# Performance work log

Hardware: AMD Instinct MI355X
Metric: run time of the kernel (lower is better)

The kernel has to match this reference:

```python
import jax, jax.numpy as jnp
import numpy as np

EPS = 1e-05


def project_to_poincare_ball(v, eps=EPS):
    # clip norm to < 1 - eps
    norm = jnp.linalg.norm(v, axis=-1, keepdims=True)
    scale = jnp.minimum((1.0 - eps) / (norm + 1e-10), 1.0)
    return v * scale


def setup_inputs() -> dict:
    key = jax.random.key(0)
    k1, k2 = jax.random.split(key)
    B, S, D, V = 2, 2048, 512, 32000
    # scale by 0.02 so typical norms (~0.45) lie inside the unit ball
    hidden_states = jax.random.normal(k1, (B, S, D), dtype=jnp.float32) * 0.02
    weight = jax.random.normal(k2, (V, D), dtype=jnp.float32) * 0.02
    return {"hidden_states": hidden_states, "weight": weight}


def reference(hidden_states, weight):
    eps = EPS
    B, S, D = hidden_states.shape
    x = hidden_states.reshape(-1, D)                 # (N, D)
    x = project_to_poincare_ball(x, eps)
    y = project_to_poincare_ball(weight, eps)        # (V, D)

    x_norm_sq = jnp.sum(x * x, axis=-1, keepdims=True)   # (N, 1)
    y_norm_sq = jnp.sum(y * y, axis=-1)                  # (V,)

    # torch.cdist(p=2, use_mm_for_euclid_dist): ||x-y|| via mm expansion,
    # clamped at 0 before sqrt. NOTE: original code names this diff_norm_sq
    # but it is the (unsquared) distance -- reproduced faithfully.
    sq = x_norm_sq + y_norm_sq[None, :] - 2.0 * (x @ y.T)   # (N, V)
    dist = jnp.sqrt(jnp.maximum(sq, 0.0))

    denom = (1.0 - x_norm_sq) * (1.0 - y_norm_sq)[None, :]  # (N, V)
    argument = 1.0 + 2.0 * dist / (denom + eps)
    argument = jnp.maximum(argument, 1.0 + eps)
    distances = jnp.arccosh(argument)                       # (N, V)

    logits = -distances
    return logits.reshape(B, S, -1)
```

## Files before the change

kernel.cpp:

```cpp
#include <hip/hip_runtime.h>
#include <hip/hip_bf16.h>

#define D_DIM 512
#define EPS 1e-5f
#define BM 256
#define BN 128
#define BK 32
#define KT 16
#define SLOT_SHORTS (BM * BK + BN * BK)

typedef __attribute__((ext_vector_type(8))) short bf16x8;
typedef __attribute__((ext_vector_type(4))) float f32x4;

__device__ __forceinline__ unsigned short f2bf(float f) {
  unsigned int u = __float_as_uint(f);
  u += 0x7FFFu + ((u >> 16) & 1u);
  return (unsigned short)(u >> 16);
}

__global__ __launch_bounds__(256) void prep_rows2(
    const float* __restrict__ x, const float* __restrict__ w,
    unsigned short* __restrict__ Xbf, unsigned short* __restrict__ Ybf,
    float* __restrict__ xnsq, float* __restrict__ ynsq, int N, int total)
{
  int row  = blockIdx.x * 4 + (threadIdx.x >> 6);
  int lane = threadIdx.x & 63;
  if (row >= total) return;

  const float* src; unsigned short* dst; float* nsq; int r;
  if (row < N) { src = x; dst = Xbf; nsq = xnsq; r = row; }
  else         { src = w; dst = Ybf; nsq = ynsq; r = row - N; }

  const float4* s = (const float4*)(src + (size_t)r * D_DIM);
  float4 v0 = s[lane];
  float4 v1 = s[lane + 64];
  float ss = v0.x*v0.x + v0.y*v0.y + v0.z*v0.z + v0.w*v0.w
           + v1.x*v1.x + v1.y*v1.y + v1.z*v1.z + v1.w*v1.w;
  #pragma unroll
  for (int off = 32; off; off >>= 1) ss += __shfl_xor(ss, off);

  float norm  = sqrtf(ss);
  float scale = fminf((1.0f - EPS) / (norm + 1e-10f), 1.0f);
  if (lane == 0) nsq[r] = ss * scale * scale;

  ushort4 o0, o1;
  o0.x = f2bf(v0.x * scale); o0.y = f2bf(v0.y * scale);
  o0.z = f2bf(v0.z * scale); o0.w = f2bf(v0.w * scale);
  o1.x = f2bf(v1.x * scale); o1.y = f2bf(v1.y * scale);
  o1.z = f2bf(v1.z * scale); o1.w = f2bf(v1.w * scale);

  ushort4* dp = (ushort4*)(dst + (size_t)r * D_DIM);
  dp[lane]      = o0;
  dp[lane + 64] = o1;
}

__global__ __launch_bounds__(512, 4) void hyp_gemm(
    const unsigned short* __restrict__ Xbf, const unsigned short* __restrict__ Ybf,
    const float* __restrict__ xnsq, const float* __restrict__ ynsq,
    float* __restrict__ out, int N, int V)
{
  __shared__ __attribute__((aligned(16))) unsigned short sAB[3][SLOT_SHORTS];

  int bid = blockIdx.x;
  int local = bid >> 3;
  int bn = local >> 1;
  int bm = (bid & 7) * 2 + (local & 1);

  int tid  = threadIdx.x;
  int wid  = tid >> 6;
  int lane = tid & 63;
  int wm = wid >> 1, wn = wid & 1;

  size_t a_row0 = (size_t)bm * BM;
  size_t b_row0 = (size_t)bn * BN;

  auto STAGE = [&](int slot, int kt) {
    int k0 = kt * BK;
    char* base = (char*)&sAB[slot][0];
    #pragma unroll
    for (int i = 0; i < 2; ++i) {
      int c = i * 512 + tid;
      int row = c >> 2;
      int s = (c & 3) ^ ((c >> 3) & 3);
      const unsigned short* gA = Xbf + (a_row0 + row) * D_DIM + k0 + s * 8;
      char* lA = base + (size_t)(i * 512 + wid * 64) * 16;
      __builtin_amdgcn_global_load_lds(
          (const __attribute__((address_space(1))) void*)gA,
          (__attribute__((address_space(3))) void*)lA, 16, 0, 0);
    }
    {
      int c = tid;
      int row = c >> 2;
      int s = (c & 3) ^ ((c >> 3) & 3);
      const unsigned short* gB = Ybf + (b_row0 + row) * D_DIM + k0 + s * 8;
      char* lB = base + (size_t)(BM * BK) * 2 + (size_t)(wid * 64) * 16;
      __builtin_amdgcn_global_load_lds(
          (const __attribute__((address_space(1))) void*)gB,
          (__attribute__((address_space(3))) void*)lB, 16, 0, 0);
    }
  };

  int jr = lane & 15;
  int h  = lane >> 4;
  float xnv[4], dxv[4];
  #pragma unroll
  for (int m = 0; m < 4; ++m) {
    float xn = xnsq[bm * BM + wm * 64 + m * 16 + jr];
    xnv[m] = xn; dxv[m] = 1.0f - xn;
  }
  f32x4 ynv[4], dyv[4];
  #pragma unroll
  for (int n = 0; n < 4; ++n) {
    f32x4 y4 = *(const f32x4*)&ynsq[bn * BN + wn * 64 + n * 16 + h * 4];
    ynv[n] = y4;
    dyv[n] = 1.0f - y4;
  }

  f32x4 acc[4][4] = {};
  int r = lane & 15;
  int slotoff = ((lane >> 4) ^ ((r >> 1) & 3)) * 8;

  STAGE(0, 0);
  STAGE(1, 1);

  #pragma unroll
  for (int t = 0; t < KT; ++t) {
    if (t == KT - 1) {
      asm volatile("s_waitcnt vmcnt(0)" ::: "memory");
    } else {
      asm volatile("s_waitcnt vmcnt(3)" ::: "memory");
    }
    __builtin_amdgcn_sched_barrier(0);
    __builtin_amdgcn_s_barrier();
    __builtin_amdgcn_sched_barrier(0);

    const unsigned short* sA = &sAB[t % 3][0];
    const unsigned short* sB = sA + BM * BK;
    bf16x8 a[4], b[4];
    #pragma unroll
    for (int m = 0; m < 4; ++m)
      a[m] = *(const bf16x8*)&sA[(wm * 64 + m * 16 + r) * BK + slotoff];
    #pragma unroll
    for (int n = 0; n < 4; ++n)
      b[n] = *(const bf16x8*)&sB[(wn * 64 + n * 16 + r) * BK + slotoff];

    if (t + 2 < KT) STAGE((t + 2) % 3, t + 2);

    #pragma unroll
    for (int m = 0; m < 4; ++m)
      #pragma unroll
      for (int n = 0; n < 4; ++n)
        acc[m][n] = __builtin_amdgcn_mfma_f32_16x16x32_bf16(b[n], a[m], acc[m][n], 0, 0, 0);
  }

  __syncthreads();
  float* epi = (float*)&sAB[0][0] + wid * (16 * 68);

  float cmv[4];
  #pragma unroll
  for (int m = 0; m < 4; ++m) cmv[m] = 2.0f * __builtin_amdgcn_rcpf(dxv[m]);
  f32x4 rdy[4];
  #pragma unroll
  for (int n = 0; n < 4; ++n) {
    #pragma unroll
    for (int q = 0; q < 4; ++q) rdy[n][q] = __builtin_amdgcn_rcpf(dyv[n][q]);
  }

  size_t out_row0 = (size_t)bm * BM + wm * 64;
  int    out_col0 = bn * BN + wn * 64;

  #pragma unroll
  for (int m = 0; m < 4; ++m) {
    float xn = xnv[m], cm = cmv[m];
    #pragma unroll
    for (int n = 0; n < 4; ++n) {
      f32x4 f;
      #pragma unroll
      for (int q = 0; q < 4; ++q) {
        float dot  = acc[m][n][q];
        float sq   = fmaxf(xn + ynv[n][q] - 2.0f * dot, 0.0f);
        float dist = __builtin_amdgcn_sqrtf(sq);
        float arg  = fmaf(dist * cm, rdy[n][q], 1.0f);
        arg = fmaxf(arg, 1.0f + EPS);
        float t2 = __builtin_amdgcn_sqrtf(fmaf(arg, arg, -1.0f));
        f[q] = -__logf(arg + t2);
      }
      *(f32x4*)&epi[jr * 68 + n * 16 + h * 4] = f;
    }
    #pragma unroll
    for (int k = 0; k < 4; ++k) {
      int xl = k * 4 + h;
      f32x4 f = *(const f32x4*)&epi[xl * 68 + jr * 4];
      size_t rg = out_row0 + m * 16 + xl;
      int    cg = out_col0 + jr * 4;
      __builtin_nontemporal_store(f, (f32x4*)(out + rg * (size_t)V + cg));
    }
  }
}

extern "C" void kernel_launch(void* const* d_in, const int* in_sizes, int n_in,
                              void* d_out, int out_size, void* d_ws, size_t ws_size,
                              hipStream_t stream) {
  const float* x = (const float*)d_in[0];
  const float* w = (const float*)d_in[1];
  float* out = (float*)d_out;

  int N = in_sizes[0] / D_DIM;
  int V = in_sizes[1] / D_DIM;

  char* ws = (char*)d_ws;
  unsigned short* Xbf = (unsigned short*)ws;
  size_t xbf_bytes = (size_t)N * D_DIM * 2;
  unsigned short* Ybf = (unsigned short*)(ws + xbf_bytes);
  size_t ybf_bytes = (size_t)V * D_DIM * 2;
  float* xnsq = (float*)(ws + xbf_bytes + ybf_bytes);
  float* ynsq = xnsq + N;

  int total = N + V;
  prep_rows2<<<dim3((total + 3) / 4), dim3(256), 0, stream>>>(
      x, w, Xbf, Ybf, xnsq, ynsq, N, total);

  int nwg = (N / BM) * (V / BN);
  hyp_gemm<<<dim3(nwg), dim3(512), 0, stream>>>(Xbf, Ybf, xnsq, ynsq, out, N, V);
}
```

Measured before the change: 228.1 us.

## Enlarge GEMM tile to 256x256 with double-buffered LDS and split MFMA phases

The output tile grows from 256x128 to 256x256, so each of the 8 warps computes a 128x64 sub-tile with 32 accumulators, raising reuse of each LDS fragment. LDS staging moves from a three-slot ring to two buffers with a one-step-ahead prefetch and a full vmcnt(0) wait each iteration. The MFMA work is split into two halves separated by barriers and s_setprio, with the second pair of B fragments loaded between them. The larger tile cuts LDS read traffic per FLOP, but it halves occupancy, makes global-load latency harder to hide, and adds extra workgroup barriers.

```diff
diff --git a/kernel.cpp b/kernel.cpp
--- a/kernel.cpp
+++ b/kernel.cpp
@@ -4,10 +4,9 @@
 #define D_DIM 512
 #define EPS 1e-5f
 #define BM 256
-#define BN 128
+#define BN 256
 #define BK 32
 #define KT 16
-#define SLOT_SHORTS (BM * BK + BN * BK)
 
 typedef __attribute__((ext_vector_type(8))) short bf16x8;
 typedef __attribute__((ext_vector_type(4))) float f32x4;
@@ -54,12 +53,12 @@
   dp[lane + 64] = o1;
 }
 
-__global__ __launch_bounds__(512, 4) void hyp_gemm(
+__global__ __launch_bounds__(512, 2) void hyp_gemm(
     const unsigned short* __restrict__ Xbf, const unsigned short* __restrict__ Ybf,
     const float* __restrict__ xnsq, const float* __restrict__ ynsq,
     float* __restrict__ out, int N, int V)
 {
-  __shared__ __attribute__((aligned(16))) unsigned short sAB[3][SLOT_SHORTS];
+  __shared__ __attribute__((aligned(16))) unsigned short regions[2][2 * BM * BK];
 
   int bid = blockIdx.x;
   int local = bid >> 3;
@@ -69,108 +68,114 @@
   int tid  = threadIdx.x;
   int wid  = tid >> 6;
   int lane = tid & 63;
-  int wm = wid >> 1, wn = wid & 1;
+  int wm = wid >> 2, wn = wid & 3;
 
   size_t a_row0 = (size_t)bm * BM;
   size_t b_row0 = (size_t)bn * BN;
 
-  auto STAGE = [&](int slot, int kt) {
+  int rA = tid >> 2;
+  int sw = (tid & 3) ^ ((tid >> 2) & 3);
+  auto STAGE = [&](int reg, int kt) {
     int k0 = kt * BK;
-    char* base = (char*)&sAB[slot][0];
-    #pragma unroll
-    for (int i = 0; i < 2; ++i) {
-      int c = i * 512 + tid;
-      int row = c >> 2;
-      int s = (c & 3) ^ ((c >> 3) & 3);
-      const unsigned short* gA = Xbf + (a_row0 + row) * D_DIM + k0 + s * 8;
-      char* lA = base + (size_t)(i * 512 + wid * 64) * 16;
+    char* base = (char*)&regions[reg][0];
+    #pragma unroll
+    for (int j = 0; j < 2; ++j) {
+      const unsigned short* g = Xbf + (a_row0 + j * 128 + rA) * D_DIM + k0 + sw * 8;
+      char* l = base + j * 8192 + wid * 1024;
       __builtin_amdgcn_global_load_lds(
-          (const __attribute__((address_space(1))) void*)gA,
-          (__attribute__((address_space(3))) void*)lA, 16, 0, 0);
-    }
-    {
-      int c = tid;
-      int row = c >> 2;
-      int s = (c & 3) ^ ((c >> 3) & 3);
-      const unsigned short* gB = Ybf + (b_row0 + row) * D_DIM + k0 + s * 8;
-      char* lB = base + (size_t)(BM * BK) * 2 + (size_t)(wid * 64) * 16;
+          (const __attribute__((address_space(1))) void*)g,
+          (__attribute__((address_space(3))) void*)l, 16, 0, 0);
+    }
+    #pragma unroll
+    for (int j = 0; j < 2; ++j) {
+      const unsigned short* g = Ybf + (b_row0 + j * 128 + rA) * D_DIM + k0 + sw * 8;
+      char* l = base + 16384 + j * 8192 + wid * 1024;
       __builtin_amdgcn_global_load_lds(
-          (const __attribute__((address_space(1))) void*)gB,
-          (__attribute__((address_space(3))) void*)lB, 16, 0, 0);
+          (const __attribute__((address_space(1))) void*)g,
+          (__attribute__((address_space(3))) void*)l, 16, 0, 0);
     }
   };
 
-  int jr = lane & 15;
-  int h  = lane >> 4;
-  float xnv[4], dxv[4];
-  #pragma unroll
-  for (int m = 0; m < 4; ++m) {
-    float xn = xnsq[bm * BM + wm * 64 + m * 16 + jr];
-    xnv[m] = xn; dxv[m] = 1.0f - xn;
-  }
-  f32x4 ynv[4], dyv[4];
+  f32x4 acc[8][4] = {};
+  int r = lane & 15;
+  int h = lane >> 4;
+  int slotoff = ((h ^ (r & 3)) * 8);
+
+  STAGE(0, 0);
+
+  #pragma unroll
+  for (int t = 0; t < KT; ++t) {
+    const unsigned short* sA = &regions[t & 1][0];
+    const unsigned short* sB = sA + BM * BK;
+
+    asm volatile("s_waitcnt vmcnt(0)" ::: "memory");
+    __builtin_amdgcn_sched_barrier(0);
+    __builtin_amdgcn_s_barrier();
+    __builtin_amdgcn_sched_barrier(0);
+
+    bf16x8 a[8], b0, b1;
+    #pragma unroll
+    for (int m = 0; m < 8; ++m)
+      a[m] = *(const bf16x8*)&sA[(wm * 128 + m * 16 + r) * BK + slotoff];
+    b0 = *(const bf16x8*)&sB[(wn * 64 + 0 * 16 + r) * BK + slotoff];
+    b1 = *(const bf16x8*)&sB[(wn * 64 + 1 * 16 + r) * BK + slotoff];
+
+    if (t + 1 < KT) STAGE((t + 1) & 1, t + 1);
+
+    __builtin_amdgcn_sched_barrier(0);
+    __builtin_amdgcn_s_barrier();
+    __builtin_amdgcn_sched_barrier(0);
+    __builtin_amdgcn_s_setprio(1);
+    #pragma unroll
+    for (int m = 0; m < 8; ++m) {
+      acc[m][0] = __builtin_amdgcn_mfma_f32_16x16x32_bf16(b0, a[m], acc[m][0], 0, 0, 0);
+      acc[m][1] = __builtin_amdgcn_mfma_f32_16x16x32_bf16(b1, a[m], acc[m][1], 0, 0, 0);
+    }
+    __builtin_amdgcn_s_setprio(0);
+
+    __builtin_amdgcn_sched_barrier(0);
+    __builtin_amdgcn_s_barrier();
+    __builtin_amdgcn_sched_barrier(0);
+    bf16x8 b2 = *(const bf16x8*)&sB[(wn * 64 + 2 * 16 + r) * BK + slotoff];
+    bf16x8 b3 = *(const bf16x8*)&sB[(wn * 64 + 3 * 16 + r) * BK + slotoff];
+
+    __builtin_amdgcn_sched_barrier(0);
+    __builtin_amdgcn_s_barrier();
+    __builtin_amdgcn_sched_barrier(0);
+    __builtin_amdgcn_s_setprio(1);
+    #pragma unroll
+    for (int m = 0; m < 8; ++m) {
+      acc[m][2] = __builtin_amdgcn_mfma_f32_16x16x32_bf16(b2, a[m], acc[m][2], 0, 0, 0);
+      acc[m][3] = __builtin_amdgcn_mfma_f32_16x16x32_bf16(b3, a[m], acc[m][3], 0, 0, 0);
+    }
+    __builtin_amdgcn_s_setprio(0);
+  }
+
+  __syncthreads();
+  float* epi = (float*)&regions[0][0] + wid * (16 * 68);
+
+  int jr = r;
+  float xnv[8], cmv[8];
+  #pragma unroll
+  for (int m = 0; m < 8; ++m) {
+    float xn = xnsq[bm * BM + wm * 128 + m * 16 + jr];
+    xnv[m] = xn;
+    cmv[m] = 2.0f * __builtin_amdgcn_rcpf(1.0f - xn);
+  }
+  f32x4 ynv[4], rdy[4];
   #pragma unroll
   for (int n = 0; n < 4; ++n) {
     f32x4 y4 = *(const f32x4*)&ynsq[bn * BN + wn * 64 + n * 16 + h * 4];
     ynv[n] = y4;
-    dyv[n] = 1.0f - y4;
-  }
-
-  f32x4 acc[4][4] = {};
-  int r = lane & 15;
-  int slotoff = ((lane >> 4) ^ ((r >> 1) & 3)) * 8;
-
-  STAGE(0, 0);
-  STAGE(1, 1);
-
-  #pragma unroll
-  for (int t = 0; t < KT; ++t) {
-    if (t == KT - 1) {
-      asm volatile("s_waitcnt vmcnt(0)" ::: "memory");
-    } else {
-      asm volatile("s_waitcnt vmcnt(3)" ::: "memory");
-    }
-    __builtin_amdgcn_sched_barrier(0);
-    __builtin_amdgcn_s_barrier();
-    __builtin_amdgcn_sched_barrier(0);
-
-    const unsigned short* sA = &sAB[t % 3][0];
-    const unsigned short* sB = sA + BM * BK;
-    bf16x8 a[4], b[4];
-    #pragma unroll
-    for (int m = 0; m < 4; ++m)
-      a[m] = *(const bf16x8*)&sA[(wm * 64 + m * 16 + r) * BK + slotoff];
-    #pragma unroll
-    for (int n = 0; n < 4; ++n)
-      b[n] = *(const bf16x8*)&sB[(wn * 64 + n * 16 + r) * BK + slotoff];
-
-    if (t + 2 < KT) STAGE((t + 2) % 3, t + 2);
-
-    #pragma unroll
-    for (int m = 0; m < 4; ++m)
-      #pragma unroll
-      for (int n = 0; n < 4; ++n)
-        acc[m][n] = __builtin_amdgcn_mfma_f32_16x16x32_bf16(b[n], a[m], acc[m][n], 0, 0, 0);
-  }
-
-  __syncthreads();
-  float* epi = (float*)&sAB[0][0] + wid * (16 * 68);
-
-  float cmv[4];
-  #pragma unroll
-  for (int m = 0; m < 4; ++m) cmv[m] = 2.0f * __builtin_amdgcn_rcpf(dxv[m]);
-  f32x4 rdy[4];
-  #pragma unroll
-  for (int n = 0; n < 4; ++n) {
-    #pragma unroll
-    for (int q = 0; q < 4; ++q) rdy[n][q] = __builtin_amdgcn_rcpf(dyv[n][q]);
-  }
-
-  size_t out_row0 = (size_t)bm * BM + wm * 64;
+    #pragma unroll
+    for (int q = 0; q < 4; ++q) rdy[n][q] = __builtin_amdgcn_rcpf(1.0f - y4[q]);
+  }
+
+  size_t out_row0 = (size_t)bm * BM + wm * 128;
   int    out_col0 = bn * BN + wn * 64;
 
   #pragma unroll
-  for (int m = 0; m < 4; ++m) {
+  for (int m = 0; m < 8; ++m) {
     float xn = xnv[m], cm = cmv[m];
     #pragma unroll
     for (int n = 0; n < 4; ++n) {
```

Measured after the change: 241.6 us. 5.9% more time.
